# Optimization experiments

Measured on AMD Instinct MI355X. Metric: run time of the kernel, lower is better.

## Reference

```python
import jax, jax.numpy as jnp
import numpy as np

WIN = (8, 7, 7)
SHIFT = (4, 3, 3)  # window_size // 2, applied on the 2nd (shifted) block
HEADS = 24
DIM = 768
RPB_SIZE = (2 * WIN[0] - 1) * (2 * WIN[1] - 1) * (2 * WIN[2] - 1)  # 2535


def rel_pos_index():
    d, h, w = WIN
    coords = np.stack(np.meshgrid(np.arange(d), np.arange(h), np.arange(w), indexing='ij')).reshape(3, -1)
    rel = (coords[:, :, None] - coords[:, None, :]).transpose(1, 2, 0)
    rel[:, :, 0] += d - 1
    rel[:, :, 1] += h - 1
    rel[:, :, 2] += w - 1
    rel[:, :, 0] *= (2 * h - 1) * (2 * w - 1)
    rel[:, :, 1] *= 2 * w - 1
    return rel.sum(-1).astype(np.int32)


def compute_mask(D, H, W):
    # static shapes -> pure numpy, traced-constant under jit
    img = np.zeros((D, H, W), np.float32)
    cnt = 0
    sl = lambda ws, ss: [slice(None, -ws), slice(-ws, -ss), slice(-ss, None)]
    for d in sl(WIN[0], SHIFT[0]):
        for h in sl(WIN[1], SHIFT[1]):
            for w in sl(WIN[2], SHIFT[2]):
                img[d, h, w] = cnt
                cnt += 1
    m = img.reshape(D // WIN[0], WIN[0], H // WIN[1], WIN[1], W // WIN[2], WIN[2])
    m = m.transpose(0, 2, 4, 1, 3, 5).reshape(-1, WIN[0] * WIN[1] * WIN[2])
    am = m[:, None, :] - m[:, :, None]
    return jnp.asarray(np.where(am != 0, -100.0, 0.0).astype(np.float32))  # (nW, N, N)


def window_partition(x):
    B, D, H, W, C = x.shape
    x = x.reshape(B, D // WIN[0], WIN[0], H // WIN[1], WIN[1], W // WIN[2], WIN[2], C)
    return x.transpose(0, 1, 3, 5, 2, 4, 6, 7).reshape(-1, WIN[0] * WIN[1] * WIN[2], C)


def window_reverse(win, B, D, H, W):
    x = win.reshape(B, D // WIN[0], H // WIN[1], W // WIN[2], WIN[0], WIN[1], WIN[2], -1)
    return x.transpose(0, 1, 4, 2, 5, 3, 6, 7).reshape(B, D, H, W, -1)


def layer_norm(x, g, b, eps=1e-5):
    mu = x.mean(-1, keepdims=True)
    var = ((x - mu) ** 2).mean(-1, keepdims=True)
    return (x - mu) * jax.lax.rsqrt(var + eps) * g + b


def gelu(x):
    return jax.nn.gelu(x, approximate=False)  # torch nn.GELU default = exact erf


def window_attention(xw, p, rpi, mask):
    Bw, N, C = xw.shape
    hd = C // HEADS
    qkv = (xw @ p['qkv_w'].T + p['qkv_b']).reshape(Bw, N, 3, HEADS, hd).transpose(2, 0, 3, 1, 4)
    q, k, v = qkv[0] * (hd ** -0.5), qkv[1], qkv[2]
    attn = jnp.einsum('bhnd,bhmd->bhnm', q, k)  # (Bw, H, N, N)
    bias = p['rpb'][rpi.reshape(-1)].reshape(N, N, HEADS).transpose(2, 0, 1)
    attn = attn + bias[None]
    if mask is not None:
        nW = mask.shape[0]
        attn = (attn.reshape(Bw // nW, nW, HEADS, N, N) + mask[None, :, None]).reshape(Bw, HEADS, N, N)
    attn = jax.nn.softmax(attn, axis=-1)
    out = jnp.einsum('bhnm,bhmd->bhnd', attn, v).transpose(0, 2, 1, 3).reshape(Bw, N, C)
    return out @ p['proj_w'].T + p['proj_b']


def swin_block(x, p, shifted, mask, rpi):
    B, D, H, W, C = x.shape
    shortcut = x
    h = layer_norm(x, p['n1_g'], p['n1_b'])
    if shifted:
        h = jnp.roll(h, (-SHIFT[0], -SHIFT[1], -SHIFT[2]), axis=(1, 2, 3))
    w = window_attention(window_partition(h), p, rpi, mask if shifted else None)
    h = window_reverse(w, B, D, H, W)
    if shifted:
        h = jnp.roll(h, SHIFT, axis=(1, 2, 3))
    x = shortcut + h
    h = layer_norm(x, p['n2_g'], p['n2_b'])
    h = gelu(h @ p['fc1_w'].T + p['fc1_b']) @ p['fc2_w'].T + p['fc2_b']
    return x + h


def _forward(x, n1_g, n1_b, qkv_w, qkv_b, proj_w, proj_b, rpb, n2_g, n2_b, fc1_w, fc1_b, fc2_w, fc2_b, hln_g, hln_b, c1_w, c1_b, c2_w, c2_b, rpi):
    B, C, D, H, W = x.shape
    mask = compute_mask(D, H, W)
    blk = dict(n1_g=n1_g, n1_b=n1_b, qkv_w=qkv_w, qkv_b=qkv_b, proj_w=proj_w, proj_b=proj_b, rpb=rpb,
               n2_g=n2_g, n2_b=n2_b, fc1_w=fc1_w, fc1_b=fc1_b, fc2_w=fc2_w, fc2_b=fc2_b)
    outs = []
    for br in range(2):  # batch1 (score) / batch2 (weight) branches
        h = x.transpose(0, 2, 3, 4, 1)  # b c d h w -> b d h w c
        for bl in range(2):  # depth=2; second block is shifted
            p = {k: v[br, bl] for k, v in blk.items()}
            h = swin_block(h, p, bl % 2 == 1, mask, rpi)
        y = layer_norm(h, hln_g[br], hln_b[br])          # nn.LayerNorm(768)
        y = gelu(jnp.einsum('bdhwc,oc->bdhwo', y, c1_w[br]) + c1_b[br])  # Conv3d 768->64 k=1 + GELU
        y = gelu(jnp.einsum('bdhwo,po->bdhwp', y, c2_w[br]) + c2_b[br])  # Conv3d 64->2 k=1 + GELU
        outs.append(y)
    return (outs[0] * outs[1]).transpose(0, 4, 1, 2, 3)  # score * weight -> (B, 2, D, H, W)


def setup_inputs():
    key = jax.random.key(0)
    ks = jax.random.split(key, 8)
    B, T, Hs, Ws = 2, 16, 14, 14
    s = 0.02
    f = lambda i, shape: jax.random.normal(ks[i], shape, jnp.float32) * s
    return dict(
        x=jax.random.normal(ks[0], (B, DIM, T, Hs, Ws), jnp.float32),
        n1_g=jnp.ones((2, 2, DIM), jnp.float32), n1_b=jnp.zeros((2, 2, DIM), jnp.float32),
        qkv_w=f(1, (2, 2, 3 * DIM, DIM)), qkv_b=jnp.zeros((2, 2, 3 * DIM), jnp.float32),
        proj_w=f(2, (2, 2, DIM, DIM)), proj_b=jnp.zeros((2, 2, DIM), jnp.float32),
        rpb=f(3, (2, 2, RPB_SIZE, HEADS)),
        n2_g=jnp.ones((2, 2, DIM), jnp.float32), n2_b=jnp.zeros((2, 2, DIM), jnp.float32),
        fc1_w=f(4, (2, 2, 4 * DIM, DIM)), fc1_b=jnp.zeros((2, 2, 4 * DIM), jnp.float32),
        fc2_w=f(5, (2, 2, DIM, 4 * DIM)), fc2_b=jnp.zeros((2, 2, DIM), jnp.float32),
        hln_g=jnp.ones((2, DIM), jnp.float32), hln_b=jnp.zeros((2, DIM), jnp.float32),
        c1_w=f(6, (2, 64, DIM)), c1_b=jnp.zeros((2, 64), jnp.float32),
        c2_w=f(7, (2, 2, 64)), c2_b=jnp.zeros((2, 2), jnp.float32),
        rpi=jnp.asarray(rel_pos_index()),
    )


def reference(x, n1_g, n1_b, qkv_w, qkv_b, proj_w, proj_b, rpb, n2_g, n2_b, fc1_w, fc1_b, fc2_w, fc2_b, hln_g, hln_b, c1_w, c1_b, c2_w, c2_b, rpi):
    return _forward(x, n1_g, n1_b, qkv_w, qkv_b, proj_w, proj_b, rpb, n2_g, n2_b, fc1_w, fc1_b, fc2_w, fc2_b, hln_g, hln_b, c1_w, c1_b, c2_w, c2_b, rpi)
```

## Files before the change

### kernel.cpp

```cpp
#include <hip/hip_runtime.h>
#include <hip/hip_bf16.h>

#define T_TOK 6272
#define CDIM  768
#define NTOK  392
#define NWIN  16
#define NHEADS 24
#define HDIM  32
#define QSCALE 0.17677669529663687f

#define NKT 26
#define NQT 25
#define KS_ST 40
#define VS_ST 456
#define PS_ST 424

typedef unsigned short ushort_t;
typedef __attribute__((ext_vector_type(8))) short bf16x8;
typedef __attribute__((ext_vector_type(4))) short bf16x4;
typedef __attribute__((ext_vector_type(4))) float f32x4;

__device__ __forceinline__ float bf2f(ushort_t h) {
    union { unsigned int u; float f; } v; v.u = ((unsigned int)h) << 16; return v.f;
}
__device__ __forceinline__ ushort_t f2bf(float f) {
    return __bfloat16_as_ushort(__float2bfloat16(f));
}
__device__ __forceinline__ float gelu_f(float x) {
    return 0.5f * x * (1.0f + erff(x * 0.70710678118654752f));
}

__device__ __forceinline__ void gload16(const ushort_t* g, ushort_t* l) {
    __builtin_amdgcn_global_load_lds(
        (const __attribute__((address_space(1))) void*)g,
        (__attribute__((address_space(3))) void*)l,
        16, 0, 0);
}

__global__ __launch_bounds__(256) void k_transpose_in(const float* __restrict__ x,
                                                      float* __restrict__ X) {
    __shared__ float tile[32][33];
    int b  = blockIdx.z;
    int s0 = blockIdx.x * 32, c0 = blockIdx.y * 32;
    int tx = threadIdx.x, ty = threadIdx.y;
#pragma unroll
    for (int r = 0; r < 4; ++r)
        tile[ty + r * 8][tx] = x[((size_t)b * 768 + c0 + ty + r * 8) * 3136 + s0 + tx];
    __syncthreads();
#pragma unroll
    for (int r = 0; r < 4; ++r)
        X[((size_t)b * 3136 + s0 + ty + r * 8) * 768 + c0 + tx] = tile[tx][ty + r * 8];
}

__global__ __launch_bounds__(256) void k_f2b(const float* __restrict__ s,
                                             ushort_t* __restrict__ d, int n4) {
    int i = blockIdx.x * 256 + threadIdx.x;
    if (i >= n4) return;
    float4 v = ((const float4*)s)[i];
    bf16x4 r;
    r[0] = (short)f2bf(v.x); r[1] = (short)f2bf(v.y);
    r[2] = (short)f2bf(v.z); r[3] = (short)f2bf(v.w);
    *(bf16x4*)&d[(size_t)i * 4] = r;
}

__global__ __launch_bounds__(256) void k_rpbT(const float* __restrict__ rpb,
                                              float* __restrict__ rpbT) {
    int idx = blockIdx.x * 256 + threadIdx.x;
    if (idx >= 24 * 2535) return;
    int h = idx / 2535, r = idx - h * 2535;
    rpbT[idx] = rpb[(size_t)r * 24 + h];
}

__global__ __launch_bounds__(256) void k_bias(const float* __restrict__ rpbT,
                                              const int* __restrict__ rpi,
                                              ushort_t* __restrict__ Bias) {
    int row = blockIdx.x;
    int h = row / 392, i = row - h * 392;
    const float* rp = rpbT + (size_t)h * 2535;
    const int* ri = rpi + (size_t)i * NTOK;
    ushort_t* out = Bias + (size_t)row * 416;
    for (int j = threadIdx.x; j < 416; j += 256) {
        float v = (j < NTOK) ? rp[ri[j]] : 0.f;
        out[j] = f2bf(v);
    }
}

__global__ __launch_bounds__(256) void k_ln_bf(const float* __restrict__ X,
                                               ushort_t* __restrict__ Y,
                                               const float* __restrict__ g,
                                               const float* __restrict__ bta,
                                               int mode) {
    int row = blockIdx.x;
    int src = row;
    if (mode != 0) {
        int wi = row / NTOK, n = row % NTOK;
        int b = wi >> 3, rem = wi & 7;
        int wd = rem >> 2, wh = (rem >> 1) & 1, ww = rem & 1;
        int dn = n / 49, r2 = n % 49, hn = r2 / 7, wn = r2 % 7;
        int d = wd * 8 + dn, h = wh * 7 + hn, w = ww * 7 + wn;
        if (mode == 2) { d = (d + 4) & 15; h = (h + 3) % 14; w = (w + 3) % 14; }
        src = (b * 16 + d) * 196 + h * 14 + w;
    }
    const float* xr = X + (size_t)src * CDIM;
    int tid = threadIdx.x;
    float v0 = xr[tid], v1 = xr[tid + 256], v2 = xr[tid + 512];
    float s = v0 + v1 + v2;
    float q = v0 * v0 + v1 * v1 + v2 * v2;
    __shared__ float red[8];
#pragma unroll
    for (int off = 32; off > 0; off >>= 1) {
        s += __shfl_down(s, off);
        q += __shfl_down(q, off);
    }
    int lane = tid & 63, wv = tid >> 6;
    if (lane == 0) { red[wv] = s; red[4 + wv] = q; }
    __syncthreads();
    float ts = red[0] + red[1] + red[2] + red[3];
    float tq = red[4] + red[5] + red[6] + red[7];
    float mu  = ts * (1.0f / 768.0f);
    float var = tq * (1.0f / 768.0f) - mu * mu;
    float rstd = rsqrtf(var + 1e-5f);
    ushort_t* yr = Y + (size_t)row * CDIM;
    yr[tid]       = f2bf((v0 - mu) * rstd * g[tid]       + bta[tid]);
    yr[tid + 256] = f2bf((v1 - mu) * rstd * g[tid + 256] + bta[tid + 256]);
    yr[tid + 512] = f2bf((v2 - mu) * rstd * g[tid + 512] + bta[tid + 512]);
}

__global__ __launch_bounds__(256) void k_ln_f32(const float* __restrict__ X,
                                                float* __restrict__ Y,
                                                const float* __restrict__ g,
                                                const float* __restrict__ bta) {
    int row = blockIdx.x, tid = threadIdx.x;
    const float* xr = X + (size_t)row * CDIM;
    float v0 = xr[tid], v1 = xr[tid + 256], v2 = xr[tid + 512];
    float s = v0 + v1 + v2;
    float q = v0 * v0 + v1 * v1 + v2 * v2;
    __shared__ float red[8];
#pragma unroll
    for (int off = 32; off > 0; off >>= 1) {
        s += __shfl_down(s, off);
        q += __shfl_down(q, off);
    }
    int lane = tid & 63, wv = tid >> 6;
    if (lane == 0) { red[wv] = s; red[4 + wv] = q; }
    __syncthreads();
    float ts = red[0] + red[1] + red[2] + red[3];
    float tq = red[4] + red[5] + red[6] + red[7];
    float mu  = ts * (1.0f / 768.0f);
    float var = tq * (1.0f / 768.0f) - mu * mu;
    float rstd = rsqrtf(var + 1e-5f);
    float* yr = Y + (size_t)row * CDIM;
    yr[tid]       = (v0 - mu) * rstd * g[tid]       + bta[tid];
    yr[tid + 256] = (v1 - mu) * rstd * g[tid + 256] + bta[tid + 256];
    yr[tid + 512] = (v2 - mu) * rstd * g[tid + 512] + bta[tid + 512];
}

__global__ __launch_bounds__(256) void k_gemm_mfma(const ushort_t* __restrict__ A,
                                                   const ushort_t* __restrict__ W,
                                                   const float* __restrict__ bias,
                                                   float* __restrict__ Cf,
                                                   ushort_t* __restrict__ Cb,
                                                   int M, int N, int K,
                                                   int act, int remap, int accum, int outbf) {
    __shared__ ushort_t As[2][128 * 32];
    __shared__ ushort_t Bs[2][128 * 32];
    int tid = threadIdx.x, lane = tid & 63, w = tid >> 6;
    int wm = w >> 1, wn = w & 1;

    int nx = gridDim.x;
    int nwg = nx * gridDim.y;
    int orig = blockIdx.y * nx + blockIdx.x;
    int sq = nwg >> 3, sr = nwg & 7;
    int xcd = orig & 7, sidx = orig >> 3;
    int swz = ((xcd < sr) ? xcd * (sq + 1) : sr * (sq + 1) + (xcd - sr) * sq) + sidx;
    int m0 = (swz / nx) * 128, n0 = (swz % nx) * 128;

    int rr = lane >> 2, ss = (lane & 3) * 8;
    const ushort_t* gA0 = A + (size_t)(m0 + w * 32 + rr) * K + ss;
    const ushort_t* gA1 = gA0 + (size_t)16 * K;
    const ushort_t* gB0 = W + (size_t)(n0 + w * 32 + rr) * K + ss;
    const ushort_t* gB1 = gB0 + (size_t)16 * K;
    int lb = (w * 32) * 32;

    f32x4 acc[4][4];
#pragma unroll
    for (int mi = 0; mi < 4; ++mi)
#pragma unroll
        for (int ni = 0; ni < 4; ++ni) acc[mi][ni] = (f32x4){0.f, 0.f, 0.f, 0.f};

    int nt = K >> 5;
    gload16(gA0, &As[0][lb]);
    gload16(gA1, &As[0][lb + 512]);
    gload16(gB0, &Bs[0][lb]);
    gload16(gB1, &Bs[0][lb + 512]);
    __syncthreads();

    int cur = 0;
    for (int t = 0; t < nt; ++t) {
        if (t + 1 < nt) {
            int k1 = (t + 1) << 5;
            gload16(gA0 + k1, &As[cur ^ 1][lb]);
            gload16(gA1 + k1, &As[cur ^ 1][lb + 512]);
            gload16(gB0 + k1, &Bs[cur ^ 1][lb]);
            gload16(gB1 + k1, &Bs[cur ^ 1][lb + 512]);
        }
        bf16x8 af[4], bg[4];
#pragma unroll
        for (int mi = 0; mi < 4; ++mi)
            af[mi] = *(const bf16x8*)&As[cur][(wm * 64 + mi * 16 + (lane & 15)) * 32 + (lane >> 4) * 8];
#pragma unroll
        for (int ni = 0; ni < 4; ++ni)
            bg[ni] = *(const bf16x8*)&Bs[cur][(wn * 64 + ni * 16 + (lane & 15)) * 32 + (lane >> 4) * 8];
#pragma unroll
        for (int mi = 0; mi < 4; ++mi)
#pragma unroll
            for (int ni = 0; ni < 4; ++ni)
                acc[mi][ni] = __builtin_amdgcn_mfma_f32_16x16x32_bf16(af[mi], bg[ni], acc[mi][ni], 0, 0, 0);
        __syncthreads();
        cur ^= 1;
    }

    int cl = lane & 15, rq = lane >> 4;
#pragma unroll
    for (int mi = 0; mi < 4; ++mi) {
#pragma unroll
        for (int ni = 0; ni < 4; ++ni) {
            int gcol = n0 + wn * 64 + ni * 16 + cl;
            float bv = bias[gcol];
#pragma unroll
            for (int i = 0; i < 4; ++i) {
                int r = m0 + wm * 64 + mi * 16 + rq * 4 + i;
                float v = acc[mi][ni][i] + bv;
                if (act) v = gelu_f(v);
                if (outbf) {
                    float sc = (outbf == 2 && gcol < 768) ? QSCALE : 1.0f;
                    Cb[(size_t)r * N + gcol] = f2bf(v * sc);
                } else {
                    size_t orow;
                    if (remap == 0) {
                        orow = (size_t)r * N;
                    } else {
                        int wi = r / NTOK, n = r % NTOK;
                        int b = wi >> 3, rem = wi & 7;
                        int wd = rem >> 2, wh = (rem >> 1) & 1, ww = rem & 1;
                        int dn = n / 49, r2 = n % 49, hn = r2 / 7, wnn = r2 % 7;
                        int d = wd * 8 + dn, h = wh * 7 + hn, ww2 = ww * 7 + wnn;
                        if (remap == 2) { d = (d + 4) & 15; h = (h + 3) % 14; ww2 = (ww2 + 3) % 14; }
                        orow = (size_t)((b * 16 + d) * 196 + h * 14 + ww2) * N;
                    }
                    if (accum) Cf[orow + gcol] += v;
                    else       Cf[orow + gcol] = v;
                }
            }
        }
    }
}

__global__ __launch_bounds__(256) void k_gemm_f32(const float* __restrict__ A,
                                                  const float* __restrict__ W,
                                                  const float* __restrict__ bias,
                                                  float* __restrict__ C,
                                                  int M, int N, int K, int act) {
    __shared__ float As[16][64];
    __shared__ float Bs[16][64];
    int tid = threadIdx.x;
    int m0 = blockIdx.y * 64, n0 = blockIdx.x * 64;
    int lrow = tid >> 2;
    int lk   = (tid & 3) * 4;
    const float* aptr = A + (size_t)(m0 + lrow) * K + lk;
    const float* wptr = W + (size_t)(n0 + lrow) * K + lk;
    int tx = tid & 15, ty = tid >> 4;
    float acc[4][4] = {};
    for (int kt = 0; kt < K; kt += 16) {
        float4 av = *(const float4*)(aptr + kt);
        float4 wv4 = *(const float4*)(wptr + kt);
        As[lk + 0][lrow] = av.x;  As[lk + 1][lrow] = av.y;
        As[lk + 2][lrow] = av.z;  As[lk + 3][lrow] = av.w;
        Bs[lk + 0][lrow] = wv4.x; Bs[lk + 1][lrow] = wv4.y;
        Bs[lk + 2][lrow] = wv4.z; Bs[lk + 3][lrow] = wv4.w;
        __syncthreads();
#pragma unroll
        for (int k = 0; k < 16; ++k) {
            float4 a = *(const float4*)&As[k][ty * 4];
            float4 b = *(const float4*)&Bs[k][tx * 4];
            float avv[4] = {a.x, a.y, a.z, a.w};
            float bvv[4] = {b.x, b.y, b.z, b.w};
#pragma unroll
            for (int i = 0; i < 4; ++i)
#pragma unroll
                for (int j = 0; j < 4; ++j)
                    acc[i][j] += avv[i] * bvv[j];
        }
        __syncthreads();
    }
    float bvals[4];
#pragma unroll
    for (int j = 0; j < 4; ++j) bvals[j] = bias[n0 + tx * 4 + j];
#pragma unroll
    for (int i = 0; i < 4; ++i) {
        int r = m0 + ty * 4 + i;
#pragma unroll
        for (int j = 0; j < 4; ++j) {
            float v = acc[i][j] + bvals[j];
            if (act) v = gelu_f(v);
            C[(size_t)r * N + n0 + tx * 4 + j] = v;
        }
    }
}

__global__ __launch_bounds__(256) void k_attn_mfma(const ushort_t* __restrict__ QKVb,
                                                   const ushort_t* __restrict__ Bias,
                                                   ushort_t* __restrict__ AO,
                                                   int shifted) {
    __shared__ int      Lrid[NTOK];
    __shared__ ushort_t Ks[NTOK * KS_ST];
    __shared__ ushort_t Vs[32 * VS_ST];
    __shared__ ushort_t Ps[4][16 * PS_ST];

    int wi   = blockIdx.x / NHEADS;
    int head = blockIdx.x % NHEADS;
    int wbase = wi * NTOK;
    int tid = threadIdx.x, lane = tid & 63, wv = tid >> 6;
    int cl = lane & 15, g = lane >> 4;
    const ushort_t* QW = QKVb + (size_t)wbase * 2304;

    for (int idx = tid; idx < NTOK * 4; idx += 256) {
        int j = idx >> 2, d8 = (idx & 3) * 8;
        const ushort_t* rowp = QW + (size_t)j * 2304 + head * 32 + d8;
        bf16x8 kv = *(const bf16x8*)(rowp + 768);
        *(bf16x8*)&Ks[j * KS_ST + d8] = kv;
        bf16x8 vv = *(const bf16x8*)(rowp + 1536);
#pragma unroll
        for (int t = 0; t < 8; ++t)
            Vs[(d8 + t) * VS_ST + j] = (ushort_t)vv[t];
    }
    for (int idx = tid; idx < 32 * 24; idx += 256) {
        int d = idx / 24, jj = idx - d * 24;
        Vs[d * VS_ST + 392 + jj] = 0;
    }
    if (shifted) {
        int rem = wi & 7;
        int wd = rem >> 2, wh = (rem >> 1) & 1, ww = rem & 1;
        for (int idx = tid; idx < NTOK; idx += 256) {
            int dn = idx / 49, r2 = idx % 49, hn = r2 / 7, wn = r2 % 7;
            int d = wd * 8 + dn, h = wh * 7 + hn, w = ww * 7 + wn;
            Lrid[idx] = (((d < 8) ? 0 : (d < 12 ? 1 : 2)) * 3 +
                         ((h < 7) ? 0 : (h < 11 ? 1 : 2))) * 3 +
                         ((w < 7) ? 0 : (w < 11 ? 1 : 2));
        }
    }
    __syncthreads();

    ushort_t* Pw = Ps[wv];
    const ushort_t* Bh = Bias + (size_t)head * 392 * 416;

    for (int qt = wv; qt < NQT; qt += 4) {
        int qrow = qt * 16 + cl; if (qrow > 391) qrow = 391;
        bf16x8 qfrag = *(const bf16x8*)(QW + (size_t)qrow * 2304 + head * 32 + g * 8);

        f32x4 acc[NKT];
#pragma unroll
        for (int kt = 0; kt < NKT; ++kt) {
            int krow = kt * 16 + cl; if (krow > 391) krow = 391;
            bf16x8 kfrag = *(const bf16x8*)&Ks[krow * KS_ST + g * 8];
            acc[kt] = __builtin_amdgcn_mfma_f32_16x16x32_bf16(
                qfrag, kfrag, (f32x4){0.f, 0.f, 0.f, 0.f}, 0, 0, 0);
        }

        int qc[4], ridq[4];
        float mrow[4];
#pragma unroll
        for (int i = 0; i < 4; ++i) {
            int qg = qt * 16 + g * 4 + i;
            qc[i] = qg > 391 ? 391 : qg;
            ridq[i] = shifted ? Lrid[qc[i]] : 0;
            mrow[i] = -1e30f;
        }
#pragma unroll
        for (int kt = 0; kt < NKT; ++kt) {
            int key = kt * 16 + cl;
            int kc = key > 391 ? 391 : key;
            int ridk = shifted ? Lrid[kc] : 0;
            bool pad = key > 391;
#pragma unroll
            for (int i = 0; i < 4; ++i) {
                float s = acc[kt][i] + bf2f(Bh[(size_t)qc[i] * 416 + key]);
                if (shifted && ridk != ridq[i]) s -= 100.0f;
                if (pad) s = -1e30f;
                acc[kt][i] = s;
                mrow[i] = fmaxf(mrow[i], s);
            }
        }
#pragma unroll
        for (int off = 1; off < 16; off <<= 1)
#pragma unroll
            for (int i = 0; i < 4; ++i)
                mrow[i] = fmaxf(mrow[i], __shfl_xor(mrow[i], off));

        float srow[4] = {0.f, 0.f, 0.f, 0.f};
#pragma unroll
        for (int kt = 0; kt < NKT; ++kt) {
            int key = kt * 16 + cl;
#pragma unroll
            for (int i = 0; i < 4; ++i) {
                float p = __expf(acc[kt][i] - mrow[i]);
                srow[i] += p;
                Pw[(g * 4 + i) * PS_ST + key] = f2bf(p);
            }
        }
#pragma unroll
        for (int off = 1; off < 16; off <<= 1)
#pragma unroll
            for (int i = 0; i < 4; ++i)
                srow[i] += __shfl_xor(srow[i], off);

        __threadfence_block();

        f32x4 out0 = (f32x4){0.f, 0.f, 0.f, 0.f};
        f32x4 out1 = (f32x4){0.f, 0.f, 0.f, 0.f};
#pragma unroll
        for (int c = 0; c < 13; ++c) {
            int ko = c * 32 + g * 8;
            bf16x8 pfrag = *(const bf16x8*)&Pw[cl * PS_ST + ko];
            bf16x8 v0 = *(const bf16x8*)&Vs[cl * VS_ST + ko];
            bf16x8 v1 = *(const bf16x8*)&Vs[(16 + cl) * VS_ST + ko];
            out0 = __builtin_amdgcn_mfma_f32_16x16x32_bf16(pfrag, v0, out0, 0, 0, 0);
            out1 = __builtin_amdgcn_mfma_f32_16x16x32_bf16(pfrag, v1, out1, 0, 0, 0);
        }

#pragma unroll
        for (int i = 0; i < 4; ++i) {
            float inv = 1.0f / srow[i];
            int qg = qt * 16 + g * 4 + i;
            if (qg < NTOK) {
                size_t ob = (size_t)(wbase + qg) * CDIM + head * 32;
                AO[ob + cl]      = f2bf(out0[i] * inv);
                AO[ob + 16 + cl] = f2bf(out1[i] * inv);
            }
        }
    }
}

__global__ __launch_bounds__(256) void k_head_c2(const float* __restrict__ Y64,
                                                 const float* __restrict__ w2,
                                                 const float* __restrict__ b2,
                                                 float* __restrict__ O2) {
    int idx = blockIdx.x * 256 + threadIdx.x;
    if (idx >= T_TOK * 2) return;
    int t = idx >> 1, p = idx & 1;
    const float* yr = Y64 + (size_t)t * 64;
    float acc = b2[p];
#pragma unroll
    for (int o = 0; o < 64; ++o) acc += yr[o] * w2[p * 64 + o];
    O2[idx] = gelu_f(acc);
}

__global__ __launch_bounds__(256) void k_final(const float* __restrict__ O2,
                                               float* __restrict__ out) {
    int idx = blockIdx.x * 256 + threadIdx.x;
    if (idx >= 2 * 2 * 3136) return;
    int b = idx / 6272;
    int p = (idx / 3136) & 1;
    int s = idx % 3136;
    int t = b * 3136 + s;
    out[idx] = O2[t * 2 + p] * O2[(size_t)T_TOK * 2 + t * 2 + p];
}

extern "C" void kernel_launch(void* const* d_in, const int* in_sizes, int n_in,
                              void* d_out, int out_size, void* d_ws, size_t ws_size,
                              hipStream_t stream) {
    const float* x     = (const float*)d_in[0];
    const float* n1_g  = (const float*)d_in[1];
    const float* n1_b  = (const float*)d_in[2];
    const float* qkv_w = (const float*)d_in[3];
    const float* qkv_b = (const float*)d_in[4];
    const float* proj_w= (const float*)d_in[5];
    const float* proj_b= (const float*)d_in[6];
    const float* rpb   = (const float*)d_in[7];
    const float* n2_g  = (const float*)d_in[8];
    const float* n2_b  = (const float*)d_in[9];
    const float* fc1_w = (const float*)d_in[10];
    const float* fc1_b = (const float*)d_in[11];
    const float* fc2_w = (const float*)d_in[12];
    const float* fc2_b = (const float*)d_in[13];
    const float* hln_g = (const float*)d_in[14];
    const float* hln_b = (const float*)d_in[15];
    const float* c1_w  = (const float*)d_in[16];
    const float* c1_b  = (const float*)d_in[17];
    const float* c2_w  = (const float*)d_in[18];
    const float* c2_b  = (const float*)d_in[19];
    const int*   rpi   = (const int*)d_in[20];

    float* ws   = (float*)d_ws;
    float* X    = ws;
    float* BIG  = X + (size_t)T_TOK * CDIM;
    float* Y64  = BIG + (size_t)T_TOK * 2304;
    float* O2   = Y64 + (size_t)T_TOK * 64;
    ushort_t* XWb = (ushort_t*)(O2 + 2 * T_TOK * 2);
    ushort_t* WB  = XWb + (size_t)T_TOK * CDIM;
    ushort_t* WBq = WB;
    ushort_t* WBp = WBq + (size_t)2304 * 768;
    ushort_t* WB1 = WBp + (size_t)768 * 768;
    ushort_t* WB2 = WB1 + (size_t)3072 * 768;
    ushort_t* BIGb = (ushort_t*)BIG;
    ushort_t* QKVb = (ushort_t*)BIG;
    ushort_t* BiasT = WB1;
    float* rpbT = Y64;

    const int NQ = 2304 * 768, NP = 768 * 768, N1 = 3072 * 768, N2 = 768 * 3072;

    for (int br = 0; br < 2; ++br) {
        k_transpose_in<<<dim3(98, 24, 2), dim3(32, 8), 0, stream>>>(x, X);
        for (int bl = 0; bl < 2; ++bl) {
            int pb = br * 2 + bl;
            int shifted = bl;
            k_f2b<<<(NQ / 4 + 255) / 256, 256, 0, stream>>>(qkv_w + (size_t)pb * NQ, WBq, NQ / 4);
            k_f2b<<<(NP / 4 + 255) / 256, 256, 0, stream>>>(proj_w + (size_t)pb * NP, WBp, NP / 4);

            k_rpbT<<<(24 * 2535 + 255) / 256, 256, 0, stream>>>(rpb + (size_t)pb * 2535 * 24, rpbT);
            k_bias<<<24 * 392, 256, 0, stream>>>(rpbT, rpi, BiasT);

            k_ln_bf<<<T_TOK, 256, 0, stream>>>(X, XWb, n1_g + pb * 768, n1_b + pb * 768, shifted ? 2 : 1);
            k_gemm_mfma<<<dim3(18, 49), 256, 0, stream>>>(XWb, WBq, qkv_b + pb * 2304,
                                                          (float*)0, QKVb,
                                                          T_TOK, 2304, 768, 0, 0, 0, 2);
            k_attn_mfma<<<NWIN * NHEADS, 256, 0, stream>>>(QKVb, BiasT, XWb, shifted);

            k_f2b<<<(N1 / 4 + 255) / 256, 256, 0, stream>>>(fc1_w + (size_t)pb * N1, WB1, N1 / 4);
            k_f2b<<<(N2 / 4 + 255) / 256, 256, 0, stream>>>(fc2_w + (size_t)pb * N2, WB2, N2 / 4);

            k_gemm_mfma<<<dim3(6, 49), 256, 0, stream>>>(XWb, WBp, proj_b + pb * 768,
                                                         X, (ushort_t*)0,
                                                         T_TOK, 768, 768, 0, shifted ? 2 : 1, 1, 0);
            k_ln_bf<<<T_TOK, 256, 0, stream>>>(X, XWb, n2_g + pb * 768, n2_b + pb * 768, 0);
            k_gemm_mfma<<<dim3(24, 49), 256, 0, stream>>>(XWb, WB1, fc1_b + pb * 3072,
                                                          (float*)0, BIGb,
                                                          T_TOK, 3072, 768, 1, 0, 0, 1);
            k_gemm_mfma<<<dim3(6, 49), 256, 0, stream>>>(BIGb, WB2, fc2_b + pb * 768,
                                                         X, (ushort_t*)0,
                                                         T_TOK, 768, 3072, 0, 0, 1, 0);
        }
        k_ln_f32<<<T_TOK, 256, 0, stream>>>(X, BIG, hln_g + br * 768, hln_b + br * 768);
        k_gemm_f32<<<dim3(1, 98), 256, 0, stream>>>(BIG, c1_w + (size_t)br * 64 * 768,
                                                    c1_b + br * 64, Y64,
                                                    T_TOK, 64, 768, 1);
        k_head_c2<<<(T_TOK * 2 + 255) / 256, 256, 0, stream>>>(Y64, c2_w + br * 128, c2_b + br * 2,
                                                               O2 + (size_t)br * T_TOK * 2);
    }
    k_final<<<(2 * 2 * 3136 + 255) / 256, 256, 0, stream>>>(O2, (float*)d_out);
}
```

Measured before the change: 1.970 ms.

## Pre-swizzle attention bias into MFMA fragment order, split query tiles, XOR-swizzle V

Bias is now precomputed per head and query tile in exactly the per-lane MFMA accumulator order, with padding keys baked in as -1e30. The attention kernel can then load four bias values with one vector load per key tile instead of four scattered global loads, and the pad check goes away. The attention grid doubles: each block handles half of the query tiles for one window and head, and block IDs are remapped to spread windows across the GPU. V stores in shared memory use an XOR swizzle to reduce bank conflicts in the transposed writes and reads. The cost is that each block now loads K and V into shared memory for only half the query work, duplicating those loads.

```diff
diff --git a/kernel.cpp b/kernel.cpp
--- a/kernel.cpp
+++ b/kernel.cpp
@@ -73,15 +73,21 @@
 
 __global__ __launch_bounds__(256) void k_bias(const float* __restrict__ rpbT,
                                               const int* __restrict__ rpi,
-                                              ushort_t* __restrict__ Bias) {
-    int row = blockIdx.x;
-    int h = row / 392, i = row - h * 392;
+                                              ushort_t* __restrict__ Bias2) {
+    int blk = blockIdx.x;
+    int h = blk / 25, qt = blk - h * 25;
     const float* rp = rpbT + (size_t)h * 2535;
-    const int* ri = rpi + (size_t)i * NTOK;
-    ushort_t* out = Bias + (size_t)row * 416;
-    for (int j = threadIdx.x; j < 416; j += 256) {
-        float v = (j < NTOK) ? rp[ri[j]] : 0.f;
-        out[j] = f2bf(v);
+    int t = threadIdx.x;
+    int i = t & 3, l = t >> 2;
+    int cl = l & 15, g = l >> 4;
+    int row = qt * 16 + g * 4 + i; if (row > 391) row = 391;
+    ushort_t* out = Bias2 + (size_t)blk * 26 * 256;
+    const int* ri = rpi + (size_t)row * NTOK;
+#pragma unroll
+    for (int kt = 0; kt < 26; ++kt) {
+        int col = kt * 16 + cl;
+        float v = (col < NTOK) ? rp[ri[col]] : -1e30f;
+        out[kt * 256 + t] = f2bf(v);
     }
 }
 
@@ -309,7 +315,7 @@
 }
 
 __global__ __launch_bounds__(256) void k_attn_mfma(const ushort_t* __restrict__ QKVb,
-                                                   const ushort_t* __restrict__ Bias,
+                                                   const ushort_t* __restrict__ Bias2,
                                                    ushort_t* __restrict__ AO,
                                                    int shifted) {
     __shared__ int      Lrid[NTOK];
@@ -317,8 +323,12 @@
     __shared__ ushort_t Vs[32 * VS_ST];
     __shared__ ushort_t Ps[4][16 * PS_ST];
 
-    int wi   = blockIdx.x / NHEADS;
-    int head = blockIdx.x % NHEADS;
+    int bid = blockIdx.x;
+    int x = bid & 7, rdec = bid >> 3;
+    int head = rdec % 24;
+    int z = rdec / 24;
+    int wi = x * 2 + (z & 1);
+    int half = z >> 1;
     int wbase = wi * NTOK;
     int tid = threadIdx.x, lane = tid & 63, wv = tid >> 6;
     int cl = lane & 15, g = lane >> 4;
@@ -330,13 +340,14 @@
         bf16x8 kv = *(const bf16x8*)(rowp + 768);
         *(bf16x8*)&Ks[j * KS_ST + d8] = kv;
         bf16x8 vv = *(const bf16x8*)(rowp + 1536);
+        int js = j ^ d8;
 #pragma unroll
         for (int t = 0; t < 8; ++t)
-            Vs[(d8 + t) * VS_ST + j] = (ushort_t)vv[t];
+            Vs[(d8 + t) * VS_ST + js] = (ushort_t)vv[t];
     }
     for (int idx = tid; idx < 32 * 24; idx += 256) {
         int d = idx / 24, jj = idx - d * 24;
-        Vs[d * VS_ST + 392 + jj] = 0;
+        Vs[d * VS_ST + ((392 + jj) ^ (d & 24))] = 0;
     }
     if (shifted) {
         int rem = wi & 7;
@@ -352,9 +363,11 @@
     __syncthreads();
 
     ushort_t* Pw = Ps[wv];
-    const ushort_t* Bh = Bias + (size_t)head * 392 * 416;
-
-    for (int qt = wv; qt < NQT; qt += 4) {
+    const ushort_t* Bh = Bias2 + (size_t)head * 25 * 26 * 256;
+    int vm0 = cl & 24, vm1 = (16 + cl) & 24;
+
+    int qend = half ? NQT : 13;
+    for (int qt = (half ? 13 : 0) + wv; qt < qend; qt += 4) {
         int qrow = qt * 16 + cl; if (qrow > 391) qrow = 391;
         bf16x8 qfrag = *(const bf16x8*)(QW + (size_t)qrow * 2304 + head * 32 + g * 8);
 
@@ -367,6 +380,7 @@
                 qfrag, kfrag, (f32x4){0.f, 0.f, 0.f, 0.f}, 0, 0, 0);
         }
 
+        const ushort_t* Bq = Bh + (size_t)qt * 26 * 256;
         int qc[4], ridq[4];
         float mrow[4];
 #pragma unroll
@@ -378,15 +392,14 @@
         }
 #pragma unroll
         for (int kt = 0; kt < NKT; ++kt) {
+            bf16x4 b4 = *(const bf16x4*)&Bq[kt * 256 + lane * 4];
             int key = kt * 16 + cl;
             int kc = key > 391 ? 391 : key;
             int ridk = shifted ? Lrid[kc] : 0;
-            bool pad = key > 391;
 #pragma unroll
             for (int i = 0; i < 4; ++i) {
-                float s = acc[kt][i] + bf2f(Bh[(size_t)qc[i] * 416 + key]);
+                float s = acc[kt][i] + bf2f((ushort_t)b4[i]);
                 if (shifted && ridk != ridq[i]) s -= 100.0f;
-                if (pad) s = -1e30f;
                 acc[kt][i] = s;
                 mrow[i] = fmaxf(mrow[i], s);
             }
@@ -422,8 +435,8 @@
         for (int c = 0; c < 13; ++c) {
             int ko = c * 32 + g * 8;
             bf16x8 pfrag = *(const bf16x8*)&Pw[cl * PS_ST + ko];
-            bf16x8 v0 = *(const bf16x8*)&Vs[cl * VS_ST + ko];
-            bf16x8 v1 = *(const bf16x8*)&Vs[(16 + cl) * VS_ST + ko];
+            bf16x8 v0 = *(const bf16x8*)&Vs[cl * VS_ST + (ko ^ vm0)];
+            bf16x8 v1 = *(const bf16x8*)&Vs[(16 + cl) * VS_ST + (ko ^ vm1)];
             out0 = __builtin_amdgcn_mfma_f32_16x16x32_bf16(pfrag, v0, out0, 0, 0, 0);
             out1 = __builtin_amdgcn_mfma_f32_16x16x32_bf16(pfrag, v1, out1, 0, 0, 0);
         }
@@ -518,13 +531,13 @@
             k_f2b<<<(NP / 4 + 255) / 256, 256, 0, stream>>>(proj_w + (size_t)pb * NP, WBp, NP / 4);
 
             k_rpbT<<<(24 * 2535 + 255) / 256, 256, 0, stream>>>(rpb + (size_t)pb * 2535 * 24, rpbT);
-            k_bias<<<24 * 392, 256, 0, stream>>>(rpbT, rpi, BiasT);
+            k_bias<<<24 * 25, 256, 0, stream>>>(rpbT, rpi, BiasT);
 
             k_ln_bf<<<T_TOK, 256, 0, stream>>>(X, XWb, n1_g + pb * 768, n1_b + pb * 768, shifted ? 2 : 1);
             k_gemm_mfma<<<dim3(18, 49), 256, 0, stream>>>(XWb, WBq, qkv_b + pb * 2304,
                                                           (float*)0, QKVb,
                                                           T_TOK, 2304, 768, 0, 0, 0, 2);
-            k_attn_mfma<<<NWIN * NHEADS, 256, 0, stream>>>(QKVb, BiasT, XWb, shifted);
+            k_attn_mfma<<<NWIN * NHEADS * 2, 256, 0, stream>>>(QKVb, BiasT, XWb, shifted);
 
             k_f2b<<<(N1 / 4 + 255) / 256, 256, 0, stream>>>(fc1_w + (size_t)pb * N1, WB1, N1 / 4);
             k_f2b<<<(N2 / 4 + 255) / 256, 256, 0, stream>>>(fc2_w + (size_t)pb * N2, WB2, N2 / 4);
```

Result: faster. 1.782 ms (-9.5%).
